# Optimization experiments

Measured on AMD Instinct MI355X. Metric: run time of the kernel, lower is better.

Reference implementation:

```python
import jax, jax.numpy as jnp
import numpy as np

EPS_NORM = 1e-12
EPS_SUM = 1e-8
NEG_BIG = -1e30


def setup_inputs() -> dict:
    key = jax.random.key(0)
    k1, k2 = jax.random.split(key)
    B, R, D = 64, 8192, 256
    reps = jax.random.normal(k1, (B, R, D), dtype=jnp.float32)
    query_rels = jax.random.randint(k2, (B,), 0, R, dtype=jnp.int64)
    return {
        "final_relation_representations": reps,
        "query_rels": query_rels,
        "similarity_threshold_raw": jnp.float32(0.8 * 2.0 - 1.0),
        "enhancement_strength_raw": jnp.float32(0.05 * 5.0 - 1.0),
        "similarity_weight_scale": jnp.float32(1.0),
        "temperature": jnp.float32(1.0),
    }


def _l2norm(x, axis):
    n = jnp.sqrt(jnp.sum(x * x, axis=axis, keepdims=True))
    return x / jnp.maximum(n, EPS_NORM)


def reference(final_relation_representations, query_rels,
              similarity_threshold_raw, enhancement_strength_raw,
              similarity_weight_scale, temperature):
    reps = final_relation_representations  # [B, R, D]
    B, R, D = reps.shape
    bidx = jnp.arange(B)
    q = jnp.clip(query_rels, 0, R - 1)  # indices assumed in range

    threshold = jax.nn.sigmoid(similarity_threshold_raw)
    strength = jax.nn.sigmoid(enhancement_strength_raw) * 0.2
    temp = jnp.clip(temperature, 0.1, 10.0)

    qrep = reps[bidx, q]  # [B, D]
    qn = _l2norm(qrep, axis=-1)
    alln = _l2norm(reps, axis=-1)
    sims = jnp.einsum('bd,brd->br', qn, alln)  # [B, R] cosine sims
    sims = sims.at[bidx, q].set(-1.0)  # exclude self

    sim_w = jax.nn.sigmoid((sims - threshold) * 10.0)  # smooth weights
    mask = sims > threshold  # == sim_w > 0.5
    has_valid = jnp.any(mask, axis=1)  # [B]

    # softmax over the valid subset only (masked)
    logits = jnp.where(mask, sims / temp, NEG_BIG)
    soft = jax.nn.softmax(logits, axis=1)

    adjusted = soft * sim_w * (1.0 + similarity_weight_scale * sims)
    adjusted = jnp.where(mask, adjusted, 0.0)
    adjusted = adjusted / (jnp.sum(adjusted, axis=1, keepdims=True) + EPS_SUM)

    weighted = jnp.einsum('br,brd->bd', adjusted, reps)  # [B, D]
    enh_q = (1.0 - strength) * qrep + strength * weighted
    enh_q = jnp.where(has_valid[:, None], enh_q, qrep)

    return reps.at[bidx, q].set(enh_q)
```

## Files before the change

### kernel.cpp

```cpp
#include <hip/hip_runtime.h>
#include <math.h>

#define EPSN 1e-12f
#define EPSS 1e-8f

__device__ __forceinline__ float wred_sum(float v) {
#pragma unroll
    for (int o = 32; o > 0; o >>= 1) v += __shfl_down(v, o, 64);
    return v;
}
__device__ __forceinline__ float wred_max(float v) {
#pragma unroll
    for (int o = 32; o > 0; o >>= 1) v = fmaxf(v, __shfl_down(v, o, 64));
    return v;
}

__device__ __forceinline__ float bred_sum(float v, float* red) {
    const int lane = threadIdx.x & 63;
    const int w = threadIdx.x >> 6;
    const int nw = blockDim.x >> 6;
    v = wred_sum(v);
    __syncthreads();
    if (lane == 0) red[w] = v;
    __syncthreads();
    float r = red[0];
    for (int i = 1; i < nw; ++i) r += red[i];
    return r;
}
__device__ __forceinline__ float bred_max(float v, float* red) {
    const int lane = threadIdx.x & 63;
    const int w = threadIdx.x >> 6;
    const int nw = blockDim.x >> 6;
    v = wred_max(v);
    __syncthreads();
    if (lane == 0) red[w] = v;
    __syncthreads();
    float r = red[0];
    for (int i = 1; i < nw; ++i) r = fmaxf(r, red[i]);
    return r;
}

__global__ __launch_bounds__(256)
void k_prep(const float* __restrict__ reps, const int* __restrict__ qrels,
            float* __restrict__ qn, int* __restrict__ qidx, int R, int D) {
    __shared__ float red[4];
    const int b = blockIdx.x;
    const int tid = threadIdx.x;
    int q = qrels[b];
    q = q < 0 ? 0 : (q >= R ? R - 1 : q);
    const size_t base = ((size_t)b * R + q) * D;
    float v = (tid < D) ? reps[base + tid] : 0.f;
    float ss = bred_sum(v * v, red);
    float n = fmaxf(sqrtf(ss), EPSN);
    if (tid < D) qn[(size_t)b * D + tid] = v / n;
    if (tid == 0) qidx[b] = q;
}

__global__ __launch_bounds__(256)
void k_copy_sims(const float* __restrict__ reps, const float* __restrict__ qn,
                 float* __restrict__ out, float* __restrict__ sims,
                 int R, int Dq , int nrows) {
    const int lane = threadIdx.x & 63;
    const int wid = threadIdx.x >> 6;
    const int row = blockIdx.x * (blockDim.x >> 6) + wid;
    if (row >= nrows) return;
    const unsigned b = (unsigned)row / (unsigned)R;
    const float4* __restrict__ src = (const float4*)reps + (size_t)row * Dq;
    float4* __restrict__ dst = (float4*)out + (size_t)row * Dq;
    const float4* __restrict__ qv = (const float4*)qn + (size_t)b * Dq;
    float dot = 0.f, ss = 0.f;
    for (int i = lane; i < Dq; i += 64) {
        float4 v = src[i];
        dst[i] = v;
        float4 qq = qv[i];
        dot += v.x * qq.x + v.y * qq.y + v.z * qq.z + v.w * qq.w;
        ss  += v.x * v.x + v.y * v.y + v.z * v.z + v.w * v.w;
    }
    dot = wred_sum(dot);
    ss  = wred_sum(ss);
    if (lane == 0) sims[row] = dot / fmaxf(sqrtf(ss), EPSN);
}

__global__ __launch_bounds__(256)
void k_epilogue(const float* __restrict__ reps, const float* __restrict__ sims_g,
                const int* __restrict__ qidx,
                const float* __restrict__ p_thr, const float* __restrict__ p_str,
                const float* __restrict__ p_scale, const float* __restrict__ p_temp,
                float* __restrict__ out, int R, int D) {
    __shared__ float s_sims[8192];
    __shared__ float s_w[2048];
    __shared__ int   s_r[2048];
    __shared__ float red[4];
    __shared__ int   s_cnt;

    const int b = blockIdx.x;
    const int tid = threadIdx.x;
    const int T = blockDim.x;
    const int q = qidx[b];

    const float threshold = 1.f / (1.f + expf(-p_thr[0]));
    const float strength  = 0.2f / (1.f + expf(-p_str[0]));
    const float scale     = p_scale[0];
    float temp = p_temp[0];
    temp = fminf(fmaxf(temp, 0.1f), 10.f);
    const float invT = 1.f / temp;

    const float* srow = sims_g + (size_t)b * R;
    float lmax = -INFINITY;
    for (int r = tid; r < R; r += T) {
        float s = srow[r];
        if (r == q) s = -1.f;
        s_sims[r] = s;
        if (s > threshold) lmax = fmaxf(lmax, s);
    }
    const float smax = bred_max(lmax, red);
    const bool has_valid = (smax > -INFINITY);
    const float m = smax * invT;

    float lz = 0.f;
    for (int r = tid; r < R; r += T) {
        float s = s_sims[r];
        if (s > threshold) lz += expf(s * invT - m);
    }
    const float Z = bred_sum(lz, red);
    const float invZ = has_valid ? (1.f / Z) : 0.f;

    float lS = 0.f;
    for (int r = tid; r < R; r += T) {
        float s = s_sims[r];
        if (s > threshold) {
            float a = expf(s * invT - m) * invZ
                    * (1.f / (1.f + expf(-(s - threshold) * 10.f)))
                    * (1.f + scale * s);
            lS += a;
        }
    }
    const float S = bred_sum(lS, red);
    const float invS = 1.f / (S + EPSS);

    float acc = 0.f;
    for (int base = 0; base < R; base += 2048) {
        if (tid == 0) s_cnt = 0;
        __syncthreads();
        int lim = base + 2048; if (lim > R) lim = R;
        for (int r = base + tid; r < lim; r += T) {
            float s = s_sims[r];
            if (s > threshold) {
                float a = expf(s * invT - m) * invZ
                        * (1.f / (1.f + expf(-(s - threshold) * 10.f)))
                        * (1.f + scale * s) * invS;
                int j = atomicAdd(&s_cnt, 1);
                s_r[j] = r;
                s_w[j] = a;
            }
        }
        __syncthreads();
        const int cnt = s_cnt;
        for (int j = 0; j < cnt; ++j)
            acc += s_w[j] * reps[((size_t)b * R + s_r[j]) * D + tid];
        __syncthreads();
    }

    if (tid < D) {
        const size_t o = ((size_t)b * R + q) * D + tid;
        const float qv = reps[o];
        out[o] = has_valid ? ((1.f - strength) * qv + strength * acc) : qv;
    }
}

extern "C" void kernel_launch(void* const* d_in, const int* in_sizes, int n_in,
                              void* d_out, int out_size, void* d_ws, size_t ws_size,
                              hipStream_t stream) {
    const float* reps   = (const float*)d_in[0];
    const int*   qrels  = (const int*)d_in[1];
    const float* p_thr  = (const float*)d_in[2];
    const float* p_str  = (const float*)d_in[3];
    const float* p_scale= (const float*)d_in[4];
    const float* p_temp = (const float*)d_in[5];
    float* out = (float*)d_out;

    const int D = 256;
    const int R = 8192;
    const int B = (int)(in_sizes[0] / ((long long)R * D));

    float* ws_sims = (float*)d_ws;
    float* ws_qn   = ws_sims + (size_t)B * R;
    int*   ws_q    = (int*)(ws_qn + (size_t)B * D);

    k_prep<<<B, 256, 0, stream>>>(reps, qrels, ws_qn, ws_q, R, D);

    const int nrows = B * R;
    const int wpb = 256 / 64;
    const int blocks = (nrows + wpb - 1) / wpb;
    k_copy_sims<<<blocks, 256, 0, stream>>>(reps, ws_qn, out, ws_sims, R, D / 4, nrows);

    k_epilogue<<<B, 256, 0, stream>>>(reps, ws_sims, ws_q, p_thr, p_str, p_scale, p_temp,
                                      out, R, D);
}
```

Measured before the change: 843.2 us.

## Fuse query normalization into copy-sims kernel with multi-row waves and nontemporal IO

Removes the separate prep kernel: each wave now recomputes the normalized query row itself and then processes 32 consecutive rows, streaming them with nontemporal loads and stores while computing cosine similarities. The epilogue merges the Z and S reductions into one pass using an algebraically equivalent denominator, and returns early when no row exceeds the threshold. This cuts one launch, the workspace round trip and one pass over shared memory, at the cost of redundant query loads per wave and the assumption that R and D are fixed compile-time constants.

```diff
diff --git a/kernel.cpp b/kernel.cpp
--- a/kernel.cpp
+++ b/kernel.cpp
@@ -3,7 +3,17 @@
 
 #define EPSN 1e-12f
 #define EPSS 1e-8f
+#define RR 8192
+#define DD 256
+#define ROWS_PER_WAVE 32
 
+typedef float f4 __attribute__((ext_vector_type(4)));
+
+__device__ __forceinline__ float wallred(float v) {
+#pragma unroll
+    for (int o = 32; o > 0; o >>= 1) v += __shfl_xor(v, o, 64);
+    return v;
+}
 __device__ __forceinline__ float wred_sum(float v) {
 #pragma unroll
     for (int o = 32; o > 0; o >>= 1) v += __shfl_down(v, o, 64);
@@ -41,53 +51,49 @@
 }
 
 __global__ __launch_bounds__(256)
-void k_prep(const float* __restrict__ reps, const int* __restrict__ qrels,
-            float* __restrict__ qn, int* __restrict__ qidx, int R, int D) {
-    __shared__ float red[4];
-    const int b = blockIdx.x;
-    const int tid = threadIdx.x;
+void k_copy_sims(const float* __restrict__ reps, const int* __restrict__ qrels,
+                 float* __restrict__ out, float* __restrict__ sims, int nrows) {
+    const int lane = threadIdx.x & 63;
+    const int wid = blockIdx.x * 4 + (threadIdx.x >> 6);
+    const long long row0 = (long long)wid * ROWS_PER_WAVE;
+    if (row0 >= nrows) return;
+    const int b = (int)(row0 >> 13);
+
     int q = qrels[b];
-    q = q < 0 ? 0 : (q >= R ? R - 1 : q);
-    const size_t base = ((size_t)b * R + q) * D;
-    float v = (tid < D) ? reps[base + tid] : 0.f;
-    float ss = bred_sum(v * v, red);
-    float n = fmaxf(sqrtf(ss), EPSN);
-    if (tid < D) qn[(size_t)b * D + tid] = v / n;
-    if (tid == 0) qidx[b] = q;
-}
+    q = q < 0 ? 0 : (q >= RR ? RR - 1 : q);
 
-__global__ __launch_bounds__(256)
-void k_copy_sims(const float* __restrict__ reps, const float* __restrict__ qn,
-                 float* __restrict__ out, float* __restrict__ sims,
-                 int R, int Dq , int nrows) {
-    const int lane = threadIdx.x & 63;
-    const int wid = threadIdx.x >> 6;
-    const int row = blockIdx.x * (blockDim.x >> 6) + wid;
-    if (row >= nrows) return;
-    const unsigned b = (unsigned)row / (unsigned)R;
-    const float4* __restrict__ src = (const float4*)reps + (size_t)row * Dq;
-    float4* __restrict__ dst = (float4*)out + (size_t)row * Dq;
-    const float4* __restrict__ qv = (const float4*)qn + (size_t)b * Dq;
-    float dot = 0.f, ss = 0.f;
-    for (int i = lane; i < Dq; i += 64) {
-        float4 v = src[i];
-        dst[i] = v;
-        float4 qq = qv[i];
-        dot += v.x * qq.x + v.y * qq.y + v.z * qq.z + v.w * qq.w;
-        ss  += v.x * v.x + v.y * v.y + v.z * v.z + v.w * v.w;
+    const f4* __restrict__ qsrc = (const f4*)(reps + ((size_t)b * RR + q) * DD);
+    f4 qv = qsrc[lane];
+    float ssq = qv.x * qv.x + qv.y * qv.y + qv.z * qv.z + qv.w * qv.w;
+    ssq = wallred(ssq);
+    const float qinv = 1.f / fmaxf(sqrtf(ssq), EPSN);
+    qv *= qinv;
+
+    const f4* __restrict__ src = (const f4*)reps + (size_t)row0 * (DD / 4);
+    f4* __restrict__ dst = (f4*)out + (size_t)row0 * (DD / 4);
+
+    float simreg = 0.f;
+#pragma unroll 4
+    for (int r = 0; r < ROWS_PER_WAVE; ++r) {
+        f4 v = __builtin_nontemporal_load(src + (size_t)r * 64 + lane);
+        __builtin_nontemporal_store(v, dst + (size_t)r * 64 + lane);
+        float dot = v.x * qv.x + v.y * qv.y + v.z * qv.z + v.w * qv.w;
+        float ss  = v.x * v.x + v.y * v.y + v.z * v.z + v.w * v.w;
+        dot = wallred(dot);
+        ss  = wallred(ss);
+        float s = dot / fmaxf(sqrtf(ss), EPSN);
+        if (lane == r) simreg = s;
     }
-    dot = wred_sum(dot);
-    ss  = wred_sum(ss);
-    if (lane == 0) sims[row] = dot / fmaxf(sqrtf(ss), EPSN);
+    if (lane < ROWS_PER_WAVE) sims[row0 + lane] = simreg;
 }
 
 __global__ __launch_bounds__(256)
 void k_epilogue(const float* __restrict__ reps, const float* __restrict__ sims_g,
-                const int* __restrict__ qidx,
+                const int* __restrict__ qrels,
                 const float* __restrict__ p_thr, const float* __restrict__ p_str,
                 const float* __restrict__ p_scale, const float* __restrict__ p_temp,
-                float* __restrict__ out, int R, int D) {
-    __shared__ float s_sims[8192];
+                float* __restrict__ out) {
+    __shared__ float s_sims[RR];
     __shared__ float s_w[2048];
     __shared__ int   s_r[2048];
     __shared__ float red[4];
@@ -95,105 +101,92 @@
 
     const int b = blockIdx.x;
     const int tid = threadIdx.x;
-    const int T = blockDim.x;
-    const int q = qidx[b];
+    int q = qrels[b];
+    q = q < 0 ? 0 : (q >= RR ? RR - 1 : q);
 
     const float threshold = 1.f / (1.f + expf(-p_thr[0]));
-    const float strength  = 0.2f / (1.f + expf(-p_str[0]));
-    const float scale     = p_scale[0];
-    float temp = p_temp[0];
-    temp = fminf(fmaxf(temp, 0.1f), 10.f);
-    const float invT = 1.f / temp;
 
-    const float* srow = sims_g + (size_t)b * R;
+    const float* __restrict__ srow = sims_g + (size_t)b * RR;
     float lmax = -INFINITY;
-    for (int r = tid; r < R; r += T) {
+    for (int r = tid; r < RR; r += DD) {
         float s = srow[r];
         if (r == q) s = -1.f;
         s_sims[r] = s;
         if (s > threshold) lmax = fmaxf(lmax, s);
     }
     const float smax = bred_max(lmax, red);
-    const bool has_valid = (smax > -INFINITY);
+    const size_t o = ((size_t)b * RR + q) * DD + tid;
+    if (!(smax > -INFINITY)) {
+        out[o] = reps[o];
+        return;
+    }
+
+    const float strength = 0.2f / (1.f + expf(-p_str[0]));
+    const float scale    = p_scale[0];
+    float temp = p_temp[0];
+    temp = fminf(fmaxf(temp, 0.1f), 10.f);
+    const float invT = 1.f / temp;
     const float m = smax * invT;
 
-    float lz = 0.f;
-    for (int r = tid; r < R; r += T) {
-        float s = s_sims[r];
-        if (s > threshold) lz += expf(s * invT - m);
-    }
-    const float Z = bred_sum(lz, red);
-    const float invZ = has_valid ? (1.f / Z) : 0.f;
-
-    float lS = 0.f;
-    for (int r = tid; r < R; r += T) {
+    float lz = 0.f, ls = 0.f;
+    for (int r = tid; r < RR; r += DD) {
         float s = s_sims[r];
         if (s > threshold) {
-            float a = expf(s * invT - m) * invZ
-                    * (1.f / (1.f + expf(-(s - threshold) * 10.f)))
-                    * (1.f + scale * s);
-            lS += a;
+            float e = expf(s * invT - m);
+            float w = 1.f / (1.f + expf(-(s - threshold) * 10.f));
+            float g = 1.f + scale * s;
+            lz += e;
+            ls += e * w * g;
         }
     }
-    const float S = bred_sum(lS, red);
-    const float invS = 1.f / (S + EPSS);
+    const float Z  = bred_sum(lz, red);
+    const float Sp = bred_sum(ls, red);
+    const float invden = 1.f / (Sp + EPSS * Z);
 
     float acc = 0.f;
-    for (int base = 0; base < R; base += 2048) {
+    for (int base = 0; base < RR; base += 2048) {
         if (tid == 0) s_cnt = 0;
         __syncthreads();
-        int lim = base + 2048; if (lim > R) lim = R;
-        for (int r = base + tid; r < lim; r += T) {
+        for (int r = base + tid; r < base + 2048; r += DD) {
             float s = s_sims[r];
             if (s > threshold) {
-                float a = expf(s * invT - m) * invZ
-                        * (1.f / (1.f + expf(-(s - threshold) * 10.f)))
-                        * (1.f + scale * s) * invS;
+                float e = expf(s * invT - m);
+                float w = 1.f / (1.f + expf(-(s - threshold) * 10.f));
+                float g = 1.f + scale * s;
                 int j = atomicAdd(&s_cnt, 1);
                 s_r[j] = r;
-                s_w[j] = a;
+                s_w[j] = e * w * g * invden;
             }
         }
         __syncthreads();
         const int cnt = s_cnt;
         for (int j = 0; j < cnt; ++j)
-            acc += s_w[j] * reps[((size_t)b * R + s_r[j]) * D + tid];
+            acc += s_w[j] * reps[((size_t)b * RR + s_r[j]) * DD + tid];
         __syncthreads();
     }
 
-    if (tid < D) {
-        const size_t o = ((size_t)b * R + q) * D + tid;
-        const float qv = reps[o];
-        out[o] = has_valid ? ((1.f - strength) * qv + strength * acc) : qv;
-    }
+    const float qv = reps[o];
+    out[o] = (1.f - strength) * qv + strength * acc;
 }
 
 extern "C" void kernel_launch(void* const* d_in, const int* in_sizes, int n_in,
                               void* d_out, int out_size, void* d_ws, size_t ws_size,
                               hipStream_t stream) {
-    const float* reps   = (const float*)d_in[0];
-    const int*   qrels  = (const int*)d_in[1];
-    const float* p_thr  = (const float*)d_in[2];
-    const float* p_str  = (const float*)d_in[3];
-    const float* p_scale= (const float*)d_in[4];
-    const float* p_temp = (const float*)d_in[5];
+    const float* reps    = (const float*)d_in[0];
+    const int*   qrels   = (const int*)d_in[1];
+    const float* p_thr   = (const float*)d_in[2];
+    const float* p_str   = (const float*)d_in[3];
+    const float* p_scale = (const float*)d_in[4];
+    const float* p_temp  = (const float*)d_in[5];
     float* out = (float*)d_out;
 
-    const int D = 256;
-    const int R = 8192;
-    const int B = (int)(in_sizes[0] / ((long long)R * D));
+    const int B = (int)(in_sizes[0] / ((long long)RR * DD));
+    float* ws_sims = (float*)d_ws;
 
-    float* ws_sims = (float*)d_ws;
-    float* ws_qn   = ws_sims + (size_t)B * R;
-    int*   ws_q    = (int*)(ws_qn + (size_t)B * D);
+    const int nrows = B * RR;
+    const int waves = nrows / ROWS_PER_WAVE;
+    const int blocks = (waves + 3) / 4;
 
-    k_prep<<<B, 256, 0, stream>>>(reps, qrels, ws_qn, ws_q, R, D);
-
-    const int nrows = B * R;
-    const int wpb = 256 / 64;
-    const int blocks = (nrows + wpb - 1) / wpb;
-    k_copy_sims<<<blocks, 256, 0, stream>>>(reps, ws_qn, out, ws_sims, R, D / 4, nrows);
-
-    k_epilogue<<<B, 256, 0, stream>>>(reps, ws_sims, ws_q, p_thr, p_str, p_scale, p_temp,
-                                      out, R, D);
+    k_copy_sims<<<blocks, 256, 0, stream>>>(reps, qrels, out, ws_sims, nrows);
+    k_epilogue<<<B, 256, 0, stream>>>(reps, ws_sims, qrels, p_thr, p_str, p_scale, p_temp, out);
 }
```

New measurement: 853.2 us. Within noise of the previous version (+1.2%).
